# Kernel tuning notes

Hardware: AMD Instinct MI355X
Metric: run time of the kernel (lower is better)

The kernel has to match this reference:

```python
import jax, jax.numpy as jnp
import numpy as np

N, E, F_IN, H = 100000, 500000, 1433, 32


def setup_inputs() -> dict:
    key = jax.random.key(0)
    ks = jax.random.split(key, 8)
    return {
        "x": jax.random.normal(ks[0], (N, F_IN), jnp.float32),
        "edge_index": jax.random.randint(ks[1], (2, E), 0, N, dtype=jnp.int32),
        "W1l": jax.random.normal(ks[2], (H, F_IN), jnp.float32) * 0.02,
        "b1l": jnp.zeros((H,), jnp.float32),
        "W1r": jax.random.normal(ks[3], (H, F_IN), jnp.float32) * 0.02,
        "W2l": jax.random.normal(ks[4], (H, H), jnp.float32) * 0.1,
        "b2l": jnp.zeros((H,), jnp.float32),
        "W2r": jax.random.normal(ks[5], (H, H), jnp.float32) * 0.1,
    }


def _sage_conv(x, src, tgt, Wl, bl, Wr, n_nodes):
    # PyG SAGEConv (mean aggr): out = lin_l(mean_{j->i} x_j) + lin_r(x_i)
    msg_sum = jax.ops.segment_sum(x[src], tgt, num_segments=n_nodes)  # [N, d]
    cnt = jax.ops.segment_sum(jnp.ones((src.shape[0],), x.dtype), tgt,
                              num_segments=n_nodes)                  # [N]
    agg = msg_sum / jnp.maximum(cnt, 1.0)[:, None]  # isolated nodes -> 0
    return agg @ Wl.T + bl + x @ Wr.T


def reference(x, edge_index, W1l, b1l, W1r, W2l, b2l, W2r):
    src, tgt = edge_index[0], edge_index[1]
    n = x.shape[0]
    h = _sage_conv(x, src, tgt, W1l, b1l, W1r, n)   # [N, 32]
    h = _sage_conv(h, src, tgt, W2l, b2l, W2r, n)   # [N, 32]
    h = jax.nn.relu(h)
    # dropout is identity in eval mode (training=False)
    return jax.nn.log_softmax(h, axis=1)
```

## Files before the change

### kernel.cpp

```cpp
#include <hip/hip_runtime.h>
#include <hip/hip_bf16.h>


typedef __attribute__((ext_vector_type(8))) __bf16 bf16x8;
typedef __attribute__((ext_vector_type(4))) float f32x4;

constexpr int K1 = 1433;
constexpr int KP1 = 1536;
constexpr int BK = 32;
constexpr int NS = 45;
constexpr int BM = 128;

__device__ __forceinline__ void gload_lds16(const void* g, void* l) {
  __builtin_amdgcn_global_load_lds(
      reinterpret_cast<const __attribute__((address_space(1))) void*>(
          reinterpret_cast<uintptr_t>(g)),
      reinterpret_cast<__attribute__((address_space(3))) void*>(
          reinterpret_cast<uintptr_t>(l)),
      16, 0, 0);
}

__device__ __forceinline__ bf16x8 cvt8(const float4 lo, const float4 hi) {
  bf16x8 r;
  r[0] = (__bf16)lo.x; r[1] = (__bf16)lo.y;
  r[2] = (__bf16)lo.z; r[3] = (__bf16)lo.w;
  r[4] = (__bf16)hi.x; r[5] = (__bf16)hi.y;
  r[6] = (__bf16)hi.z; r[7] = (__bf16)hi.w;
  return r;
}

constexpr int CONV_BLOCKS = (64 * KP1 + 64 * 32 + 255) / 256;

__global__ __launch_bounds__(256) void conv_hist(
    const float* __restrict__ W1l, const float* __restrict__ W1r,
    const float* __restrict__ W2l, const float* __restrict__ W2r,
    __bf16* __restrict__ wb1, __bf16* __restrict__ wb2,
    const int* __restrict__ ei, int* __restrict__ deg, int E) {
  if ((int)blockIdx.x < CONV_BLOCKS) {
    const int t = blockIdx.x * 256 + threadIdx.x;
    if (t < 64 * KP1) {
      const int c = t / KP1, k = t - c * KP1;
      float v = 0.0f;
      if (k < K1)
        v = (c < 32) ? W1l[(long)c * K1 + k] : W1r[(long)(c - 32) * K1 + k];
      wb1[t] = (__bf16)v;
    } else {
      const int u = t - 64 * KP1;
      if (u < 64 * 32) {
        const int c = u >> 5, k = u & 31;
        const float v = (c < 32) ? W2l[c * 32 + k] : W2r[(c - 32) * 32 + k];
        wb2[u] = (__bf16)v;
      }
    }
  } else {
    const int e = (blockIdx.x - CONV_BLOCKS) * 256 + threadIdx.x;
    if (e < E) atomicAdd(&deg[ei[E + e]], 1);
  }
}

__global__ __launch_bounds__(256) void gemm_big(const float* __restrict__ X,
                                                const __bf16* __restrict__ WB,
                                                __bf16* __restrict__ yl,
                                                float* __restrict__ yr,
                                                int Nrows) {
  __shared__ float ldsA[2][BM][BK];
  __shared__ __bf16 ldsB[2][64][BK];
  const int tid = threadIdx.x;
  const int w = tid >> 6, l = tid & 63;
  const int lr = l & 15, lg = l >> 4;
  const int row0 = blockIdx.x * BM;

  const int aRowIn = (l >> 3);
  const int aChunk = (l & 7) ^ aRowIn;
  long aRow[4];
#pragma unroll
  for (int i = 0; i < 4; ++i) {
    long r = (long)row0 + w * 32 + i * 8 + aRowIn;
    if (r >= Nrows) r = Nrows - 1;
    aRow[i] = r;
  }
  const float* const pAmax = X + (size_t)Nrows * K1 - 4;
  const int bRow = w * 16 + (l >> 2);
  const int bChunk = (l & 3) ^ ((l >> 3) & 3);
  const __bf16* const pB0 = WB + (long)bRow * KP1 + bChunk * 8;

  auto stage = [&](int s, int buf) {
    const int k0 = s * BK;
#pragma unroll
    for (int i = 0; i < 4; ++i) {
      const float* g = X + aRow[i] * K1 + k0 + aChunk * 4;
      if (g > pAmax) g = pAmax;
      gload_lds16(g, &ldsA[buf][w * 32 + i * 8][0]);
    }
    gload_lds16(pB0 + k0, &ldsB[buf][w * 16][0]);
  };

  f32x4 acc[2][4];
#pragma unroll
  for (int t = 0; t < 2; ++t)
#pragma unroll
    for (int j = 0; j < 4; ++j) acc[t][j] = (f32x4){0.f, 0.f, 0.f, 0.f};

  const int swzA = lr & 7;
  const int swzB = (lr >> 1) & 3;

  stage(0, 0);
#pragma unroll 1
  for (int s = 0; s < NS; ++s) {
    const int buf = s & 1;
    if (s + 1 < NS) {
      stage(s + 1, buf ^ 1);
      asm volatile("s_waitcnt vmcnt(5)" ::: "memory");
    } else {
      asm volatile("s_waitcnt vmcnt(0)" ::: "memory");
    }
    __builtin_amdgcn_s_barrier();
    __builtin_amdgcn_sched_barrier(0);
    bf16x8 bfrag[4];
#pragma unroll
    for (int ct = 0; ct < 4; ++ct) {
      const int br = ct * 16 + lr;
      bfrag[ct] = *reinterpret_cast<const bf16x8*>(
          &ldsB[buf][br][(lg ^ swzB) * 8]);
    }
#pragma unroll
    for (int t = 0; t < 2; ++t) {
      const int fr = w * 32 + t * 16 + lr;
      const float4 u = *reinterpret_cast<const float4*>(
          &ldsA[buf][fr][((lg * 2 + 0) ^ swzA) * 4]);
      const float4 v = *reinterpret_cast<const float4*>(
          &ldsA[buf][fr][((lg * 2 + 1) ^ swzA) * 4]);
      const bf16x8 af = cvt8(u, v);
#pragma unroll
      for (int ct = 0; ct < 4; ++ct)
        acc[t][ct] =
            __builtin_amdgcn_mfma_f32_16x16x32_bf16(af, bfrag[ct], acc[t][ct], 0, 0, 0);
    }
    __builtin_amdgcn_sched_barrier(0);
    __builtin_amdgcn_s_barrier();
  }

#pragma unroll
  for (int t = 0; t < 2; ++t) {
#pragma unroll
    for (int j = 0; j < 4; ++j) {
      const long R = (long)row0 + w * 32 + t * 16 + lg * 4 + j;
      if (R < Nrows) {
#pragma unroll
        for (int ct = 0; ct < 2; ++ct)
          yl[R * 32 + ct * 16 + lr] = (__bf16)acc[t][ct][j];
#pragma unroll
        for (int ct = 2; ct < 4; ++ct)
          yr[R * 32 + (ct - 2) * 16 + lr] = acc[t][ct][j];
      }
    }
  }
}


__global__ __launch_bounds__(256) void scan_tilesum(const int* __restrict__ deg,
                                                    int* __restrict__ tileSum,
                                                    int n) {
  __shared__ int s[256];
  const int b = blockIdx.x, t = threadIdx.x;
  const int base = b * 2048 + t * 8;
  int v = 0;
#pragma unroll
  for (int j = 0; j < 8; ++j) {
    const int i = base + j;
    if (i < n) v += deg[i];
  }
  s[t] = v;
  __syncthreads();
  for (int d = 128; d > 0; d >>= 1) {
    if (t < d) s[t] += s[t + d];
    __syncthreads();
  }
  if (t == 0) tileSum[b] = s[0];
}

__global__ __launch_bounds__(256) void scan_offsets(const int* __restrict__ deg,
                                                    const int* __restrict__ tileSum,
                                                    int* __restrict__ off,
                                                    int n, int nT) {
  __shared__ int warpTot[4];
  __shared__ int tileOffS;
  const int b = blockIdx.x, t = threadIdx.x;
  if (t < 64) {
    int v = (t < b && t < nT) ? tileSum[t] : 0;
#pragma unroll
    for (int d = 1; d < 64; d <<= 1) v += __shfl_xor(v, d);
    if (t == 0) tileOffS = v;
  }
  const int base = b * 2048 + t * 8;
  int v[8];
  int s = 0;
#pragma unroll
  for (int j = 0; j < 8; ++j) {
    const int i = base + j;
    v[j] = (i < n) ? deg[i] : 0;
    s += v[j];
  }
  const int l = t & 63, w = t >> 6;
  int inc = s;
#pragma unroll
  for (int d = 1; d < 64; d <<= 1) {
    const int o = __shfl_up(inc, d);
    if (l >= d) inc += o;
  }
  if (l == 63) warpTot[w] = inc;
  __syncthreads();
  int wo = 0;
  for (int k = 0; k < w; ++k) wo += warpTot[k];
  int ex = wo + (inc - s) + tileOffS;
#pragma unroll
  for (int j = 0; j < 8; ++j) {
    const int i = base + j;
    if (i < n) {
      off[i] = ex;
      ex += v[j];
    }
  }
}

__global__ __launch_bounds__(256) void scatter_src(const int* __restrict__ ei,
                                                   const int* __restrict__ off,
                                                   int* __restrict__ fill,
                                                   int* __restrict__ ssrc,
                                                   int E) {
  const int e = blockIdx.x * 256 + threadIdx.x;
  if (e < E) {
    const int t = ei[E + e];
    const int p = off[t] + atomicAdd(&fill[t], 1);
    ssrc[p] = ei[e];
  }
}

__global__ __launch_bounds__(256) void agg_gemm2(
    const int* __restrict__ off, const int* __restrict__ deg,
    const int* __restrict__ ssrc, const __bf16* __restrict__ yl1,
    const float* __restrict__ yr1, const float* __restrict__ b1,
    const __bf16* __restrict__ WB2, __bf16* __restrict__ yl2,
    float* __restrict__ yr2, int N) {
  __shared__ __bf16 hs[64][40];
  const int tid = threadIdx.x;
  const int nb0 = blockIdx.x * 64;
  const int c = tid & 31, r8 = tid >> 5;

  int stA[8], dgA[8];
#pragma unroll
  for (int j = 0; j < 8; ++j) {
    const int i = nb0 + r8 * 8 + j;
    stA[j] = (i < N) ? off[i] : 0;
    dgA[j] = (i < N) ? deg[i] : 0;
  }
#pragma unroll 1
  for (int j = 0; j < 8; ++j) {
    const int i = nb0 + r8 * 8 + j;
    float hv = 0.0f;
    if (i < N) {
      const int st = stA[j], d = dgA[j];
      float acc = 0.0f;
      int e = 0;
      for (; e + 4 <= d; e += 4) {
        const int s0 = ssrc[st + e + 0];
        const int s1 = ssrc[st + e + 1];
        const int s2 = ssrc[st + e + 2];
        const int s3 = ssrc[st + e + 3];
        acc += (float)yl1[(long)s0 * 32 + c] + (float)yl1[(long)s1 * 32 + c] +
               (float)yl1[(long)s2 * 32 + c] + (float)yl1[(long)s3 * 32 + c];
      }
      for (; e < d; ++e) acc += (float)yl1[(long)ssrc[st + e] * 32 + c];
      hv = acc / fmaxf((float)d, 1.0f) + b1[c] + yr1[(long)i * 32 + c];
    }
    hs[r8 * 8 + j][c] = (__bf16)hv;
  }
  __syncthreads();

  const int w = tid >> 6, l = tid & 63;
  const int lr = l & 15, lg = l >> 4;
  const bf16x8 af = *reinterpret_cast<const bf16x8*>(&hs[w * 16 + lr][lg * 8]);
  f32x4 acc4[4];
#pragma unroll
  for (int j = 0; j < 4; ++j) acc4[j] = (f32x4){0.f, 0.f, 0.f, 0.f};
#pragma unroll
  for (int ct = 0; ct < 4; ++ct) {
    const bf16x8 bf = *reinterpret_cast<const bf16x8*>(
        WB2 + (ct * 16 + lr) * 32 + lg * 8);
    acc4[ct] = __builtin_amdgcn_mfma_f32_16x16x32_bf16(af, bf, acc4[ct], 0, 0, 0);
  }
#pragma unroll
  for (int j = 0; j < 4; ++j) {
    const long R = (long)nb0 + w * 16 + lg * 4 + j;
    if (R < N) {
#pragma unroll
      for (int ct = 0; ct < 2; ++ct)
        yl2[R * 32 + ct * 16 + lr] = (__bf16)acc4[ct][j];
#pragma unroll
      for (int ct = 2; ct < 4; ++ct)
        yr2[R * 32 + (ct - 2) * 16 + lr] = acc4[ct][j];
    }
  }
}

__global__ __launch_bounds__(256) void agg_final(
    const int* __restrict__ off, const int* __restrict__ deg,
    const int* __restrict__ ssrc, const __bf16* __restrict__ yl2,
    const float* __restrict__ yr2, const float* __restrict__ bias,
    float* __restrict__ out, int N) {
  const int t = blockIdx.x * 256 + threadIdx.x;
  const int i = t >> 5, c = t & 31;
  if (i >= N) return;
  const int st = off[i], d = deg[i];
  float acc = 0.0f;
  int e = 0;
  for (; e + 4 <= d; e += 4) {
    const int s0 = ssrc[st + e + 0];
    const int s1 = ssrc[st + e + 1];
    const int s2 = ssrc[st + e + 2];
    const int s3 = ssrc[st + e + 3];
    acc += (float)yl2[(long)s0 * 32 + c] + (float)yl2[(long)s1 * 32 + c] +
           (float)yl2[(long)s2 * 32 + c] + (float)yl2[(long)s3 * 32 + c];
  }
  for (; e < d; ++e) acc += (float)yl2[(long)ssrc[st + e] * 32 + c];
  const float mean = acc / fmaxf((float)d, 1.0f);
  float v = mean + bias[c] + yr2[(long)i * 32 + c];
  v = fmaxf(v, 0.0f);
  float m = v;
#pragma unroll
  for (int dd = 16; dd >= 1; dd >>= 1) m = fmaxf(m, __shfl_xor(m, dd));
  const float ex = __expf(v - m);
  float s = ex;
#pragma unroll
  for (int dd = 16; dd >= 1; dd >>= 1) s += __shfl_xor(s, dd);
  out[(long)i * 32 + c] = (v - m) - __logf(s);
}

extern "C" void kernel_launch(void* const* d_in, const int* in_sizes, int n_in,
                              void* d_out, int out_size, void* d_ws,
                              size_t ws_size, hipStream_t stream) {
  const float* x = (const float*)d_in[0];
  const int* ei = (const int*)d_in[1];
  const float* W1l = (const float*)d_in[2];
  const float* b1l = (const float*)d_in[3];
  const float* W1r = (const float*)d_in[4];
  const float* W2l = (const float*)d_in[5];
  const float* b2l = (const float*)d_in[6];
  const float* W2r = (const float*)d_in[7];
  float* out = (float*)d_out;

  const int N = in_sizes[0] / K1;
  const int E = in_sizes[1] / 2;
  const int nTiles = (N + 2047) / 2048;

  char* ws = (char*)d_ws;
  size_t o = 0;
  auto alloc = [&](size_t bytes) {
    void* p = ws + o;
    o += (bytes + 255) & ~(size_t)255;
    return p;
  };
  __bf16* yl1 = (__bf16*)alloc((size_t)N * 32 * 2);
  float* yr1 = (float*)alloc((size_t)N * 32 * 4);
  __bf16* yl2 = (__bf16*)alloc((size_t)N * 32 * 2);
  float* yr2 = (float*)alloc((size_t)N * 32 * 4);
  __bf16* wb1 = (__bf16*)alloc((size_t)64 * KP1 * 2);
  __bf16* wb2 = (__bf16*)alloc((size_t)64 * 32 * 2);
  int* deg = (int*)alloc((size_t)2 * N * 4);
  int* fill = deg + N;
  int* off = (int*)alloc((size_t)N * 4);
  int* ssrc = (int*)alloc((size_t)E * 4);
  int* tileSum = (int*)alloc(64 * 4);

  (void)hipMemsetAsync(deg, 0, (size_t)2 * N * 4, stream);
  conv_hist<<<CONV_BLOCKS + (E + 255) / 256, 256, 0, stream>>>(
      W1l, W1r, W2l, W2r, wb1, wb2, ei, deg, E);
  scan_tilesum<<<nTiles, 256, 0, stream>>>(deg, tileSum, N);
  scan_offsets<<<nTiles, 256, 0, stream>>>(deg, tileSum, off, N, nTiles);
  scatter_src<<<(E + 255) / 256, 256, 0, stream>>>(ei, off, fill, ssrc, E);

  gemm_big<<<(N + BM - 1) / BM, 256, 0, stream>>>(x, wb1, yl1, yr1, N);
  agg_gemm2<<<(N + 63) / 64, 256, 0, stream>>>(off, deg, ssrc, yl1, yr1, b1l,
                                               wb2, yl2, yr2, N);
  agg_final<<<(N * 32 + 255) / 256, 256, 0, stream>>>(off, deg, ssrc, yl2,
                                                      yr2, b2l, out, N);
}
```

Baseline: 284.1 us.

## Fold memset, histogram and scan kernels into fewer launches

The memset now runs inside the weight-conversion kernel. The degree histogram moves into extra blocks of the big GEMM launch, where it can overlap with the memory-bound GEMM. The two scan kernels merge into one that uses an atomic counter and a spin-wait grid barrier to exchange tile sums. This cuts launch count and serialization but depends on all scan blocks being co-resident for the spin barrier.

```diff
diff --git a/kernel.cpp b/kernel.cpp
--- a/kernel.cpp
+++ b/kernel.cpp
@@ -10,6 +10,7 @@
 constexpr int BK = 32;
 constexpr int NS = 45;
 constexpr int BM = 128;
+constexpr int CONV_BLOCKS = (64 * KP1 + 64 * 32 + 255) / 256;
 
 __device__ __forceinline__ void gload_lds16(const void* g, void* l) {
   __builtin_amdgcn_global_load_lds(
@@ -29,13 +30,11 @@
   return r;
 }
 
-constexpr int CONV_BLOCKS = (64 * KP1 + 64 * 32 + 255) / 256;
-
-__global__ __launch_bounds__(256) void conv_hist(
+__global__ __launch_bounds__(256) void conv_zero(
     const float* __restrict__ W1l, const float* __restrict__ W1r,
     const float* __restrict__ W2l, const float* __restrict__ W2r,
     __bf16* __restrict__ wb1, __bf16* __restrict__ wb2,
-    const int* __restrict__ ei, int* __restrict__ deg, int E) {
+    int* __restrict__ zbuf, int zcount) {
   if ((int)blockIdx.x < CONV_BLOCKS) {
     const int t = blockIdx.x * 256 + threadIdx.x;
     if (t < 64 * KP1) {
@@ -53,8 +52,12 @@
       }
     }
   } else {
-    const int e = (blockIdx.x - CONV_BLOCKS) * 256 + threadIdx.x;
-    if (e < E) atomicAdd(&deg[ei[E + e]], 1);
+    const int base = (blockIdx.x - CONV_BLOCKS) * 4096 + threadIdx.x * 16;
+#pragma unroll
+    for (int j = 0; j < 16; ++j) {
+      const int i = base + j;
+      if (i < zcount) zbuf[i] = 0;
+    }
   }
 }
 
@@ -62,9 +65,20 @@
                                                 const __bf16* __restrict__ WB,
                                                 __bf16* __restrict__ yl,
                                                 float* __restrict__ yr,
-                                                int Nrows) {
+                                                int Nrows, int gemmBlocks,
+                                                const int* __restrict__ ei,
+                                                int* __restrict__ deg, int E) {
   __shared__ float ldsA[2][BM][BK];
   __shared__ __bf16 ldsB[2][64][BK];
+  if ((int)blockIdx.x >= gemmBlocks) {
+    const int base = ((int)blockIdx.x - gemmBlocks) * 1024 + threadIdx.x;
+#pragma unroll
+    for (int j = 0; j < 4; ++j) {
+      const int e = base + j * 256;
+      if (e < E) atomicAdd(&deg[ei[E + e]], 1);
+    }
+    return;
+  }
   const int tid = threadIdx.x;
   const int w = tid >> 6, l = tid & 63;
   const int lr = l & 15, lg = l >> 4;
@@ -157,41 +171,14 @@
   }
 }
 
-
-__global__ __launch_bounds__(256) void scan_tilesum(const int* __restrict__ deg,
-                                                    int* __restrict__ tileSum,
-                                                    int n) {
-  __shared__ int s[256];
-  const int b = blockIdx.x, t = threadIdx.x;
-  const int base = b * 2048 + t * 8;
-  int v = 0;
-#pragma unroll
-  for (int j = 0; j < 8; ++j) {
-    const int i = base + j;
-    if (i < n) v += deg[i];
-  }
-  s[t] = v;
-  __syncthreads();
-  for (int d = 128; d > 0; d >>= 1) {
-    if (t < d) s[t] += s[t + d];
-    __syncthreads();
-  }
-  if (t == 0) tileSum[b] = s[0];
-}
-
-__global__ __launch_bounds__(256) void scan_offsets(const int* __restrict__ deg,
-                                                    const int* __restrict__ tileSum,
-                                                    int* __restrict__ off,
-                                                    int n, int nT) {
+__global__ __launch_bounds__(256) void csr_scan(const int* __restrict__ deg,
+                                                int* __restrict__ tileSum,
+                                                int* __restrict__ cnt,
+                                                int* __restrict__ off, int n,
+                                                int nT) {
   __shared__ int warpTot[4];
   __shared__ int tileOffS;
   const int b = blockIdx.x, t = threadIdx.x;
-  if (t < 64) {
-    int v = (t < b && t < nT) ? tileSum[t] : 0;
-#pragma unroll
-    for (int d = 1; d < 64; d <<= 1) v += __shfl_xor(v, d);
-    if (t == 0) tileOffS = v;
-  }
   const int base = b * 2048 + t * 8;
   int v[8];
   int s = 0;
@@ -210,9 +197,30 @@
   }
   if (l == 63) warpTot[w] = inc;
   __syncthreads();
+  const int blockTot = warpTot[0] + warpTot[1] + warpTot[2] + warpTot[3];
   int wo = 0;
   for (int k = 0; k < w; ++k) wo += warpTot[k];
-  int ex = wo + (inc - s) + tileOffS;
+  if (t == 0) {
+    __hip_atomic_store(&tileSum[b], blockTot, __ATOMIC_RELEASE,
+                       __HIP_MEMORY_SCOPE_AGENT);
+    atomicAdd(cnt, 1);
+    while (__hip_atomic_load(cnt, __ATOMIC_ACQUIRE,
+                             __HIP_MEMORY_SCOPE_AGENT) < nT) {
+    }
+  }
+  __syncthreads();
+  int tv = 0;
+  if (t < 64) {
+    int x2 = (t < b) ? __hip_atomic_load(&tileSum[t], __ATOMIC_ACQUIRE,
+                                         __HIP_MEMORY_SCOPE_AGENT)
+                     : 0;
+#pragma unroll
+    for (int d = 1; d < 64; d <<= 1) x2 += __shfl_xor(x2, d);
+    tv = x2;
+  }
+  if (t == 0) tileOffS = tv;
+  __syncthreads();
+  int ex = tileOffS + wo + (inc - s);
 #pragma unroll
   for (int j = 0; j < 8; ++j) {
     const int i = base + j;
@@ -366,20 +374,23 @@
   float* yr2 = (float*)alloc((size_t)N * 32 * 4);
   __bf16* wb1 = (__bf16*)alloc((size_t)64 * KP1 * 2);
   __bf16* wb2 = (__bf16*)alloc((size_t)64 * 32 * 2);
-  int* deg = (int*)alloc((size_t)2 * N * 4);
+  int* deg = (int*)alloc((size_t)(2 * N + 64) * 4);
   int* fill = deg + N;
+  int* cnt = deg + 2 * N;
   int* off = (int*)alloc((size_t)N * 4);
   int* ssrc = (int*)alloc((size_t)E * 4);
   int* tileSum = (int*)alloc(64 * 4);
 
-  (void)hipMemsetAsync(deg, 0, (size_t)2 * N * 4, stream);
-  conv_hist<<<CONV_BLOCKS + (E + 255) / 256, 256, 0, stream>>>(
-      W1l, W1r, W2l, W2r, wb1, wb2, ei, deg, E);
-  scan_tilesum<<<nTiles, 256, 0, stream>>>(deg, tileSum, N);
-  scan_offsets<<<nTiles, 256, 0, stream>>>(deg, tileSum, off, N, nTiles);
+  const int zcount = 2 * N + 64;
+  const int zBlocks = (zcount + 4095) / 4096;
+  conv_zero<<<CONV_BLOCKS + zBlocks, 256, 0, stream>>>(W1l, W1r, W2l, W2r,
+                                                       wb1, wb2, deg, zcount);
+  const int gemmBlocks = (N + BM - 1) / BM;
+  const int histBlocks = (E + 1023) / 1024;
+  gemm_big<<<gemmBlocks + histBlocks, 256, 0, stream>>>(
+      x, wb1, yl1, yr1, N, gemmBlocks, ei, deg, E);
+  csr_scan<<<nTiles, 256, 0, stream>>>(deg, tileSum, cnt, off, N, nTiles);
   scatter_src<<<(E + 255) / 256, 256, 0, stream>>>(ei, off, fill, ssrc, E);
-
-  gemm_big<<<(N + BM - 1) / BM, 256, 0, stream>>>(x, wb1, yl1, yr1, N);
   agg_gemm2<<<(N + 63) / 64, 256, 0, stream>>>(off, deg, ssrc, yl1, yr1, b1l,
                                                wb2, yl2, yr2, N);
   agg_final<<<(N * 32 + 255) / 256, 256, 0, stream>>>(off, deg, ssrc, yl2,
```

Result: faster. 265.6 us (median of 2 runs) (-6.5%).
